# Kernel optimization log

Hardware: AMD Instinct MI355X
Metric: run time of the kernel (lower is better)

The kernel has to match this reference:

```python
import jax, jax.numpy as jnp
import numpy as np

N, M, D = 1024, 1024, 512


def setup_inputs() -> dict:
    key = jax.random.key(0)
    ks = jax.random.split(key, 12)
    s = 1.0 / np.sqrt(D)
    return {
        "q": jax.random.normal(ks[0], (N, D), jnp.float32),
        "k": jax.random.normal(ks[1], (M, D), jnp.float32),
        "v": jax.random.normal(ks[2], (M, D), jnp.float32),
        "mask": jax.random.randint(ks[3], (N, M), 0, 2) > 0,
        "Wq": jax.random.normal(ks[4], (D, D), jnp.float32) * s,
        "bq": jax.random.normal(ks[5], (D,), jnp.float32) * s,
        "Wk": jax.random.normal(ks[6], (D, D), jnp.float32) * s,
        "bk": jax.random.normal(ks[7], (D,), jnp.float32) * s,
        "Wv": jax.random.normal(ks[8], (D, D), jnp.float32) * s,
        "bv": jax.random.normal(ks[9], (D,), jnp.float32) * s,
        "Ww": jax.random.normal(ks[10], (D,), jnp.float32) * s,
        "bw": jax.random.normal(ks[11], (1,), jnp.float32) * s,
    }


def reference(q, k, v, mask, Wq, bq, Wk, bk, Wv, bv, Ww, bw):
    # Linear projections (torch Linear: x @ W.T + b)
    qp = q @ Wq.T + bq  # [N, D]
    kp = k @ Wk.T + bk  # [M, D]
    vp = v @ Wv.T + bv  # [M, D]
    # Bahdanau additive score: W(tanh(q_n + k_m)) -> [N, M]
    h = jnp.tanh(qp[:, None, :] + kp[None, :, :])  # [N, M, D]
    scores = jnp.einsum('nmd,d->nm', h, Ww) + bw[0]
    scores = jnp.where(mask, scores, jnp.float32(-1000000.0))
    attn = jax.nn.softmax(scores, axis=1)  # softmax over M (dim 1)
    context = jnp.einsum('nm,md->nd', attn, vp)  # [N, D]
    return context
```

## Files before the change

kernel.cpp:

```cpp
#include <hip/hip_runtime.h>
#include <hip/hip_bf16.h>
#include <float.h>


#define NROWS 1024
#define DDIM  512
#define MDIM  1024

typedef __attribute__((ext_vector_type(8))) short s8v;
typedef __attribute__((ext_vector_type(4))) float f4v;
typedef __attribute__((ext_vector_type(2))) float v2f;

__device__ __forceinline__ float bf2f(ushort h) {
    return __uint_as_float(((unsigned)h) << 16);
}
__device__ __forceinline__ ushort2 f2bf2(float a, float b) {
    __hip_bfloat162 t = __float22bfloat162_rn(float2{a, b});
    union { __hip_bfloat162 v; ushort2 u; } c; c.v = t;
    return c.u;
}
__device__ __forceinline__ void hl2(float a, float b, ushort2& h, ushort2& l) {
    h = f2bf2(a, b);
    l = f2bf2(a - bf2f(h.x), b - bf2f(h.y));
}

__global__ __launch_bounds__(256) void proj_gemm(
    const float* __restrict__ q, const float* __restrict__ kk_,
    const float* __restrict__ v,
    const float* __restrict__ Wq, const float* __restrict__ bq,
    const float* __restrict__ Wk, const float* __restrict__ bk,
    const float* __restrict__ Wv, const float* __restrict__ bv,
    float* __restrict__ eq, float* __restrict__ ekT,
    ushort* __restrict__ vph, ushort* __restrict__ vpl,
    float* __restrict__ rsum, float CS)
{
    __shared__ ushort Ah[2][4096], Al[2][4096], Bh[2][2048], Bl[2][2048];

    const float* A; const float* B; const float* bias;
    int biasRow;
    if (blockIdx.z == 0)      { A = q;   B = Wq;  bias = bq; biasRow = 0; }
    else if (blockIdx.z == 1) { A = Wk;  B = kk_; bias = bk; biasRow = 1; }
    else                      { A = Wv;  B = v;   bias = bv; biasRow = 1; }

    const int bx = blockIdx.x;
    const int bi = (blockIdx.z == 0) ? (bx >> 4) : (bx >> 5);
    const int bj = (blockIdx.z == 0) ? (bx & 15) : (bx & 31);

    const int t    = threadIdx.x;
    const int lane = t & 63;
    const int w    = t >> 6;
    const int lm   = lane & 15;
    const int lq   = lane >> 4;
    const int i0   = bi * 64;
    const int j0   = bj * 32;
    const int mh   = (w >> 1) * 32;
    const int nh   = (w & 1) * 16;

    if (blockIdx.z == 0 && bx == 0) {
        float4 zz = {0.f, 0.f, 0.f, 0.f};
        *(float4*)&rsum[t * 4] = zz;
    }

    const int sr = t >> 4, sc4 = t & 15;

    float4 pa[4], pb[2];

#define LOAD_CHUNK(KC)                                                         \
    {                                                                          \
        const int k0 = (KC) * 64;                                              \
        _Pragma("unroll")                                                      \
        for (int p = 0; p < 4; ++p)                                            \
            pa[p] = *(const float4*)&A[(size_t)(i0 + sr + p * 16) * DDIM       \
                                       + k0 + sc4 * 4];                        \
        _Pragma("unroll")                                                      \
        for (int p = 0; p < 2; ++p)                                            \
            pb[p] = *(const float4*)&B[(size_t)(j0 + sr + p * 16) * DDIM       \
                                       + k0 + sc4 * 4];                        \
    }

#define WRITE_CHUNK(BUF)                                                       \
    {                                                                          \
        _Pragma("unroll")                                                      \
        for (int p = 0; p < 4; ++p) {                                          \
            int r = sr + p * 16;                                               \
            int ad = r * 64 + (((sc4 >> 1) ^ (r & 7)) << 3) + (sc4 & 1) * 4;   \
            ushort2 h01, l01, h23, l23;                                        \
            hl2(pa[p].x, pa[p].y, h01, l01);                                   \
            hl2(pa[p].z, pa[p].w, h23, l23);                                   \
            ushort4 ha = {h01.x, h01.y, h23.x, h23.y};                         \
            ushort4 la = {l01.x, l01.y, l23.x, l23.y};                         \
            *(ushort4*)&Ah[BUF][ad] = ha;                                      \
            *(ushort4*)&Al[BUF][ad] = la;                                      \
        }                                                                      \
        _Pragma("unroll")                                                      \
        for (int p = 0; p < 2; ++p) {                                          \
            int r = sr + p * 16;                                               \
            int ad = r * 64 + (((sc4 >> 1) ^ (r & 7)) << 3) + (sc4 & 1) * 4;   \
            ushort2 h01, l01, h23, l23;                                        \
            hl2(pb[p].x, pb[p].y, h01, l01);                                   \
            hl2(pb[p].z, pb[p].w, h23, l23);                                   \
            ushort4 hb = {h01.x, h01.y, h23.x, h23.y};                         \
            ushort4 lb = {l01.x, l01.y, l23.x, l23.y};                         \
            *(ushort4*)&Bh[BUF][ad] = hb;                                      \
            *(ushort4*)&Bl[BUF][ad] = lb;                                      \
        }                                                                      \
    }

    f4v acc[2] = {{0.f,0.f,0.f,0.f},{0.f,0.f,0.f,0.f}};

    LOAD_CHUNK(0)
    WRITE_CHUNK(0)
    LOAD_CHUNK(1)
    __syncthreads();

    for (int kc = 0; kc < 8; ++kc) {
        const int buf = kc & 1;
#pragma unroll
        for (int ks = 0; ks < 2; ++ks) {
            const int kb = ks * 4 + lq;
            s8v afh[2], afl[2], bfh, bfl;
#pragma unroll
            for (int g = 0; g < 2; ++g) {
                int ra = mh + g * 16 + lm;
                int aa = ra * 64 + ((kb ^ (ra & 7)) << 3);
                afh[g] = *(const s8v*)&Ah[buf][aa];
                afl[g] = *(const s8v*)&Al[buf][aa];
            }
            {
                int rb = nh + lm;
                int ab = rb * 64 + ((kb ^ (rb & 7)) << 3);
                bfh = *(const s8v*)&Bh[buf][ab];
                bfl = *(const s8v*)&Bl[buf][ab];
            }
#pragma unroll
            for (int mi = 0; mi < 2; ++mi) {
                acc[mi] = __builtin_amdgcn_mfma_f32_16x16x32_bf16(
                    afh[mi], bfh, acc[mi], 0, 0, 0);
                acc[mi] = __builtin_amdgcn_mfma_f32_16x16x32_bf16(
                    afh[mi], bfl, acc[mi], 0, 0, 0);
                acc[mi] = __builtin_amdgcn_mfma_f32_16x16x32_bf16(
                    afl[mi], bfh, acc[mi], 0, 0, 0);
            }
        }
        if (kc < 7) {
            WRITE_CHUNK(buf ^ 1)
        }
        if (kc < 6) {
            LOAD_CHUNK(kc + 2)
        }
        __syncthreads();
    }

    const float CLAMP = 8192.0f;
    const float SCw   = 1.220703125e-4f;
#pragma unroll
    for (int mi = 0; mi < 2; ++mi) {
#pragma unroll
        for (int p = 0; p < 4; ++p) {
            int row = i0 + mh + mi * 16 + lq * 4 + p;
            int col = j0 + nh + lm;
            float val = acc[mi][p] + (biasRow ? bias[row] : bias[col]);
            if (blockIdx.z == 0) {
                eq[(size_t)row * 512 + col] =
                    fminf(__builtin_amdgcn_exp2f(val * CS), CLAMP) * SCw;
            } else if (blockIdx.z == 1) {
                ekT[(size_t)row * 1024 + col] =
                    fminf(__builtin_amdgcn_exp2f(val * CS), CLAMP);
            } else {
                ushort2 h2 = f2bf2(val, val);
                vph[(size_t)row * 1024 + col] = h2.x;
                ushort2 l2 = f2bf2(val - bf2f(h2.x), 0.f);
                vpl[(size_t)row * 1024 + col] = l2.x;
            }
        }
    }
#undef LOAD_CHUNK
#undef WRITE_CHUNK
}


#define TREE8(K0,K1,K2,K3,K4,K5,K6,K7,DCQ)                                     \
    {                                                                          \
        float4 wgA = *(const float4*)&wws[(DCQ)];                              \
        float4 wgB = *(const float4*)&wws[(DCQ) + 4];                          \
        _Pragma("unroll")                                                      \
        for (int nn = 0; nn < 4; ++nn) {                                       \
            float4 egA = *(const float4*)&es[nn * 512 + (DCQ)];                \
            float4 egB = *(const float4*)&es[nn * 512 + (DCQ) + 4];            \
            v2f A0 = __builtin_elementwise_fma(K0, (v2f){egA.x, egA.x}, cc2);  \
            v2f A1 = __builtin_elementwise_fma(K1, (v2f){egA.y, egA.y}, cc2);  \
            v2f A2 = __builtin_elementwise_fma(K2, (v2f){egA.z, egA.z}, cc2);  \
            v2f A3 = __builtin_elementwise_fma(K3, (v2f){egA.w, egA.w}, cc2);  \
            v2f A4 = __builtin_elementwise_fma(K4, (v2f){egB.x, egB.x}, cc2);  \
            v2f A5 = __builtin_elementwise_fma(K5, (v2f){egB.y, egB.y}, cc2);  \
            v2f A6 = __builtin_elementwise_fma(K6, (v2f){egB.z, egB.z}, cc2);  \
            v2f A7 = __builtin_elementwise_fma(K7, (v2f){egB.w, egB.w}, cc2);  \
            v2f n01 = __builtin_elementwise_fma((v2f){wgA.y, wgA.y}, A0,       \
                                                (v2f){wgA.x, wgA.x} * A1);     \
            v2f d01 = A0 * A1;                                                 \
            v2f n23 = __builtin_elementwise_fma((v2f){wgA.w, wgA.w}, A2,       \
                                                (v2f){wgA.z, wgA.z} * A3);     \
            v2f d23 = A2 * A3;                                                 \
            v2f n45 = __builtin_elementwise_fma((v2f){wgB.y, wgB.y}, A4,       \
                                                (v2f){wgB.x, wgB.x} * A5);     \
            v2f d45 = A4 * A5;                                                 \
            v2f n67 = __builtin_elementwise_fma((v2f){wgB.w, wgB.w}, A6,       \
                                                (v2f){wgB.z, wgB.z} * A7);     \
            v2f d67 = A6 * A7;                                                 \
            v2f nA = __builtin_elementwise_fma(n01, d23, n23 * d01);           \
            v2f dA = d01 * d23;                                                \
            v2f nB = __builtin_elementwise_fma(n45, d67, n67 * d45);           \
            v2f dB = d45 * d67;                                                \
            v2f num = __builtin_elementwise_fma(nA, dB, nB * dA);              \
            v2f den = dA * dB;                                                 \
            v2f r = {__builtin_amdgcn_rcpf(den.x),                             \
                     __builtin_amdgcn_rcpf(den.y)};                            \
            acc[nn] = __builtin_elementwise_fma(num, r, acc[nn]);              \
        }                                                                      \
    }

__global__ __launch_bounds__(256) void score_kernel(const float* __restrict__ eq,
                                                    const float* __restrict__ ekT,
                                                    const float* __restrict__ Ww,
                                                    const int* __restrict__ mask,
                                                    ushort* __restrict__ Ph,
                                                    ushort* __restrict__ Pl,
                                                    float* __restrict__ rsum)
{
    __shared__ __align__(16) float es[4 * 512];
    __shared__ __align__(16) float wws[512];
    const int t    = threadIdx.x;
    const int lane = t & 63;
    const int w    = t >> 6;
    const int mw   = blockIdx.x * 512 + w * 128;
    const int n0   = blockIdx.y * 4;

    const float SC = 1.220703125e-4f;

#pragma unroll
    for (int p = 0; p < 2; ++p) {
        int idx = t + p * 256;
        int nl = idx >> 7, c4 = idx & 127;
        *(float4*)&es[nl * 512 + c4 * 4] =
            *(const float4*)&eq[(size_t)(n0 + nl) * DDIM + c4 * 4];
    }
    wws[t]       = Ww[t] * SC;
    wws[t + 256] = Ww[t + 256] * SC;

    const float* gk = ekT + mw + lane * 2;

    v2f a0 = *(const v2f*)(gk + (size_t)0 * MDIM);
    v2f a1 = *(const v2f*)(gk + (size_t)1 * MDIM);
    v2f a2 = *(const v2f*)(gk + (size_t)2 * MDIM);
    v2f a3 = *(const v2f*)(gk + (size_t)3 * MDIM);
    v2f a4 = *(const v2f*)(gk + (size_t)4 * MDIM);
    v2f a5 = *(const v2f*)(gk + (size_t)5 * MDIM);
    v2f a6 = *(const v2f*)(gk + (size_t)6 * MDIM);
    v2f a7 = *(const v2f*)(gk + (size_t)7 * MDIM);

    __syncthreads();

    v2f acc[4] = {};
    const v2f cc2 = {1.220703125e-4f, 1.220703125e-4f};

    for (int dc = 0; dc < 512; dc += 16) {
        const float* g8 = gk + (size_t)(dc + 8) * MDIM;
        v2f b0 = *(const v2f*)(g8 + (size_t)0 * MDIM);
        v2f b1 = *(const v2f*)(g8 + (size_t)1 * MDIM);
        v2f b2 = *(const v2f*)(g8 + (size_t)2 * MDIM);
        v2f b3 = *(const v2f*)(g8 + (size_t)3 * MDIM);
        v2f b4 = *(const v2f*)(g8 + (size_t)4 * MDIM);
        v2f b5 = *(const v2f*)(g8 + (size_t)5 * MDIM);
        v2f b6 = *(const v2f*)(g8 + (size_t)6 * MDIM);
        v2f b7 = *(const v2f*)(g8 + (size_t)7 * MDIM);

        TREE8(a0, a1, a2, a3, a4, a5, a6, a7, dc)

        if (dc + 16 < 512) {
            const float* g16 = gk + (size_t)(dc + 16) * MDIM;
            a0 = *(const v2f*)(g16 + (size_t)0 * MDIM);
            a1 = *(const v2f*)(g16 + (size_t)1 * MDIM);
            a2 = *(const v2f*)(g16 + (size_t)2 * MDIM);
            a3 = *(const v2f*)(g16 + (size_t)3 * MDIM);
            a4 = *(const v2f*)(g16 + (size_t)4 * MDIM);
            a5 = *(const v2f*)(g16 + (size_t)5 * MDIM);
            a6 = *(const v2f*)(g16 + (size_t)6 * MDIM);
            a7 = *(const v2f*)(g16 + (size_t)7 * MDIM);
        }

        TREE8(b0, b1, b2, b3, b4, b5, b6, b7, dc + 8)
    }

    const float C2 = -2.8853900817779268f;
    const int m = mw + lane * 2;
    float rs[4];
#pragma unroll
    for (int nn = 0; nn < 4; ++nn) {
        int n = n0 + nn;
        int2 mk = *(const int2*)&mask[(size_t)n * MDIM + m];
        float p0 = mk.x ? __builtin_amdgcn_exp2f(acc[nn].x * C2) : 0.f;
        float p1 = mk.y ? __builtin_amdgcn_exp2f(acc[nn].y * C2) : 0.f;
        ushort2 h, l;
        hl2(p0, p1, h, l);
        *(ushort2*)&Ph[(size_t)n * MDIM + m] = h;
        *(ushort2*)&Pl[(size_t)n * MDIM + m] = l;
        rs[nn] = p0 + p1;
    }
#pragma unroll
    for (int off = 32; off; off >>= 1) {
        rs[0] += __shfl_xor(rs[0], off);
        rs[1] += __shfl_xor(rs[1], off);
        rs[2] += __shfl_xor(rs[2], off);
        rs[3] += __shfl_xor(rs[3], off);
    }
    if (lane == 0) {
#pragma unroll
        for (int nn = 0; nn < 4; ++nn)
            atomicAdd(&rsum[n0 + nn], rs[nn]);
    }
}

__global__ __launch_bounds__(256) void ctx_gemm(const ushort* __restrict__ Ph,
                                                const ushort* __restrict__ Pl,
                                                const ushort* __restrict__ vph,
                                                const ushort* __restrict__ vpl,
                                                const float* __restrict__ rsum,
                                                float* __restrict__ out)
{
    __shared__ __align__(16) float red[3 * 64 * 4];
    const int t    = threadIdx.x;
    const int lane = t & 63;
    const int w    = t >> 6;
    const int lm   = lane & 15;
    const int lq   = lane >> 4;
    const int d0   = blockIdx.x * 16;
    const int n0   = blockIdx.y * 16;
    const int mb   = w * 256;

    const ushort* pAh = Ph  + (size_t)(n0 + lm) * MDIM + mb + lq * 8;
    const ushort* pAl = Pl  + (size_t)(n0 + lm) * MDIM + mb + lq * 8;
    const ushort* pBh = vph + (size_t)(d0 + lm) * MDIM + mb + lq * 8;
    const ushort* pBl = vpl + (size_t)(d0 + lm) * MDIM + mb + lq * 8;

    f4v acc = {0.f, 0.f, 0.f, 0.f};
#pragma unroll 4
    for (int m0 = 0; m0 < 256; m0 += 32) {
        s8v ah = *(const s8v*)(pAh + m0);
        s8v al = *(const s8v*)(pAl + m0);
        s8v bh = *(const s8v*)(pBh + m0);
        s8v bl = *(const s8v*)(pBl + m0);
        acc = __builtin_amdgcn_mfma_f32_16x16x32_bf16(ah, bh, acc, 0, 0, 0);
        acc = __builtin_amdgcn_mfma_f32_16x16x32_bf16(ah, bl, acc, 0, 0, 0);
        acc = __builtin_amdgcn_mfma_f32_16x16x32_bf16(al, bh, acc, 0, 0, 0);
    }

    if (w > 0) *(f4v*)&red[((w - 1) * 64 + lane) * 4] = acc;
    __syncthreads();
    if (w == 0) {
#pragma unroll
        for (int i = 0; i < 3; ++i)
            acc += *(const f4v*)&red[(i * 64 + lane) * 4];
#pragma unroll
        for (int p = 0; p < 4; ++p) {
            int nrow = n0 + lq * 4 + p;
            float inv = __builtin_amdgcn_rcpf(rsum[nrow]);
            out[(size_t)nrow * DDIM + d0 + lm] = acc[p] * inv;
        }
    }
}

extern "C" void kernel_launch(void* const* d_in, const int* in_sizes, int n_in,
                              void* d_out, int out_size, void* d_ws, size_t ws_size,
                              hipStream_t stream)
{
    const float* q    = (const float*)d_in[0];
    const float* k    = (const float*)d_in[1];
    const float* v    = (const float*)d_in[2];
    const int*   mask = (const int*)d_in[3];
    const float* Wq   = (const float*)d_in[4];
    const float* bq   = (const float*)d_in[5];
    const float* Wk   = (const float*)d_in[6];
    const float* bk   = (const float*)d_in[7];
    const float* Wv   = (const float*)d_in[8];
    const float* bv   = (const float*)d_in[9];
    const float* Ww   = (const float*)d_in[10];

    float* ws    = (float*)d_ws;
    float* eq    = ws;
    float* ekT   = ws + 524288;
    ushort* vph  = (ushort*)(ws + 1048576);
    ushort* vpl  = (ushort*)(ws + 1310720);
    ushort* Ph   = (ushort*)(ws + 1572864);
    ushort* Pl   = (ushort*)(ws + 2097152);
    float* rsum  = ws + 2621440;
    float* out   = (float*)d_out;

    const float CS = 2.8853900817779268f;

    proj_gemm<<<dim3(256, 1, 3), dim3(256), 0, stream>>>(q, k, v, Wq, bq, Wk, bk,
                                                         Wv, bv, eq, ekT,
                                                         vph, vpl, rsum, CS);
    score_kernel<<<dim3(2, 256), dim3(256), 0, stream>>>(eq, ekT, Ww, mask,
                                                         Ph, Pl, rsum);
    ctx_gemm<<<dim3(32, 64), dim3(256), 0, stream>>>(Ph, Pl, vph, vpl, rsum, out);
}
```

Baseline: 175.8 us.

## Split D reduction across two wave groups in score kernel with LDS combine

The score kernel now launches 512 threads per block. Two groups of four waves each handle half of the D dimension for the same m columns, and their partial accumulators are combined through shared memory before the exp, mask and store epilogue. This doubles the waves per block and halves the serial reduction loop per thread, aiming for more latency hiding in the score computation. It costs an extra LDS buffer, a block-wide barrier, and half the waves idling during the epilogue.

Result: no change. 172.9 us (-1.6%).

```diff
diff --git a/kernel.cpp b/kernel.cpp
--- a/kernel.cpp
+++ b/kernel.cpp
@@ -219,7 +219,7 @@
         }                                                                      \
     }
 
-__global__ __launch_bounds__(256) void score_kernel(const float* __restrict__ eq,
+__global__ __launch_bounds__(512) void score_kernel(const float* __restrict__ eq,
                                                     const float* __restrict__ ekT,
                                                     const float* __restrict__ Ww,
                                                     const int* __restrict__ mask,
@@ -229,25 +229,26 @@
 {
     __shared__ __align__(16) float es[4 * 512];
     __shared__ __align__(16) float wws[512];
+    __shared__ __align__(16) float red[4 * 8 * 64];
     const int t    = threadIdx.x;
     const int lane = t & 63;
     const int w    = t >> 6;
-    const int mw   = blockIdx.x * 512 + w * 128;
+    const int mg   = w & 3;
+    const int dh   = w >> 2;
+    const int mw   = blockIdx.x * 512 + mg * 128;
     const int n0   = blockIdx.y * 4;
+    const int db   = dh * 256;
 
     const float SC = 1.220703125e-4f;
 
-#pragma unroll
-    for (int p = 0; p < 2; ++p) {
-        int idx = t + p * 256;
-        int nl = idx >> 7, c4 = idx & 127;
+    {
+        int nl = t >> 7, c4 = t & 127;
         *(float4*)&es[nl * 512 + c4 * 4] =
             *(const float4*)&eq[(size_t)(n0 + nl) * DDIM + c4 * 4];
     }
-    wws[t]       = Ww[t] * SC;
-    wws[t + 256] = Ww[t + 256] * SC;
-
-    const float* gk = ekT + mw + lane * 2;
+    wws[t] = Ww[t] * SC;
+
+    const float* gk = ekT + (size_t)db * MDIM + mw + lane * 2;
 
     v2f a0 = *(const v2f*)(gk + (size_t)0 * MDIM);
     v2f a1 = *(const v2f*)(gk + (size_t)1 * MDIM);
@@ -263,7 +264,7 @@
     v2f acc[4] = {};
     const v2f cc2 = {1.220703125e-4f, 1.220703125e-4f};
 
-    for (int dc = 0; dc < 512; dc += 16) {
+    for (int dc = 0; dc < 256; dc += 16) {
         const float* g8 = gk + (size_t)(dc + 8) * MDIM;
         v2f b0 = *(const v2f*)(g8 + (size_t)0 * MDIM);
         v2f b1 = *(const v2f*)(g8 + (size_t)1 * MDIM);
@@ -274,9 +275,9 @@
         v2f b6 = *(const v2f*)(g8 + (size_t)6 * MDIM);
         v2f b7 = *(const v2f*)(g8 + (size_t)7 * MDIM);
 
-        TREE8(a0, a1, a2, a3, a4, a5, a6, a7, dc)
-
-        if (dc + 16 < 512) {
+        TREE8(a0, a1, a2, a3, a4, a5, a6, a7, db + dc)
+
+        if (dc + 16 < 256) {
             const float* g16 = gk + (size_t)(dc + 16) * MDIM;
             a0 = *(const v2f*)(g16 + (size_t)0 * MDIM);
             a1 = *(const v2f*)(g16 + (size_t)1 * MDIM);
@@ -288,35 +289,51 @@
             a7 = *(const v2f*)(g16 + (size_t)7 * MDIM);
         }
 
-        TREE8(b0, b1, b2, b3, b4, b5, b6, b7, dc + 8)
-    }
-
-    const float C2 = -2.8853900817779268f;
-    const int m = mw + lane * 2;
-    float rs[4];
-#pragma unroll
-    for (int nn = 0; nn < 4; ++nn) {
-        int n = n0 + nn;
-        int2 mk = *(const int2*)&mask[(size_t)n * MDIM + m];
-        float p0 = mk.x ? __builtin_amdgcn_exp2f(acc[nn].x * C2) : 0.f;
-        float p1 = mk.y ? __builtin_amdgcn_exp2f(acc[nn].y * C2) : 0.f;
-        ushort2 h, l;
-        hl2(p0, p1, h, l);
-        *(ushort2*)&Ph[(size_t)n * MDIM + m] = h;
-        *(ushort2*)&Pl[(size_t)n * MDIM + m] = l;
-        rs[nn] = p0 + p1;
-    }
-#pragma unroll
-    for (int off = 32; off; off >>= 1) {
-        rs[0] += __shfl_xor(rs[0], off);
-        rs[1] += __shfl_xor(rs[1], off);
-        rs[2] += __shfl_xor(rs[2], off);
-        rs[3] += __shfl_xor(rs[3], off);
-    }
-    if (lane == 0) {
-#pragma unroll
-        for (int nn = 0; nn < 4; ++nn)
-            atomicAdd(&rsum[n0 + nn], rs[nn]);
+        TREE8(b0, b1, b2, b3, b4, b5, b6, b7, db + dc + 8)
+    }
+
+    if (dh) {
+        float* rb = &red[(mg * 8) * 64 + lane];
+        rb[0 * 64] = acc[0].x; rb[1 * 64] = acc[0].y;
+        rb[2 * 64] = acc[1].x; rb[3 * 64] = acc[1].y;
+        rb[4 * 64] = acc[2].x; rb[5 * 64] = acc[2].y;
+        rb[6 * 64] = acc[3].x; rb[7 * 64] = acc[3].y;
+    }
+    __syncthreads();
+    if (!dh) {
+        const float* rb = &red[(mg * 8) * 64 + lane];
+        acc[0].x += rb[0 * 64]; acc[0].y += rb[1 * 64];
+        acc[1].x += rb[2 * 64]; acc[1].y += rb[3 * 64];
+        acc[2].x += rb[4 * 64]; acc[2].y += rb[5 * 64];
+        acc[3].x += rb[6 * 64]; acc[3].y += rb[7 * 64];
+
+        const float C2 = -2.8853900817779268f;
+        const int m = mw + lane * 2;
+        float rs[4];
+#pragma unroll
+        for (int nn = 0; nn < 4; ++nn) {
+            int n = n0 + nn;
+            int2 mk = *(const int2*)&mask[(size_t)n * MDIM + m];
+            float p0 = mk.x ? __builtin_amdgcn_exp2f(acc[nn].x * C2) : 0.f;
+            float p1 = mk.y ? __builtin_amdgcn_exp2f(acc[nn].y * C2) : 0.f;
+            ushort2 h, l;
+            hl2(p0, p1, h, l);
+            *(ushort2*)&Ph[(size_t)n * MDIM + m] = h;
+            *(ushort2*)&Pl[(size_t)n * MDIM + m] = l;
+            rs[nn] = p0 + p1;
+        }
+#pragma unroll
+        for (int off = 32; off; off >>= 1) {
+            rs[0] += __shfl_xor(rs[0], off);
+            rs[1] += __shfl_xor(rs[1], off);
+            rs[2] += __shfl_xor(rs[2], off);
+            rs[3] += __shfl_xor(rs[3], off);
+        }
+        if (lane == 0) {
+#pragma unroll
+            for (int nn = 0; nn < 4; ++nn)
+                atomicAdd(&rsum[n0 + nn], rs[nn]);
+        }
     }
 }
 
@@ -400,7 +417,7 @@
     proj_gemm<<<dim3(256, 1, 3), dim3(256), 0, stream>>>(q, k, v, Wq, bq, Wk, bk,
                                                          Wv, bv, eq, ekT,
                                                          vph, vpl, rsum, CS);
-    score_kernel<<<dim3(2, 256), dim3(256), 0, stream>>>(eq, ekT, Ww, mask,
+    score_kernel<<<dim3(2, 256), dim3(512), 0, stream>>>(eq, ekT, Ww, mask,
                                                          Ph, Pl, rsum);
     ctx_gemm<<<dim3(32, 64), dim3(256), 0, stream>>>(Ph, Pl, vph, vpl, rsum, out);
 }
```

## Split score kernel D reduction across wave pairs with 4-wide m per lane

Applied to the files above, without the earlier changes.

Each wave now computes 4 adjacent m columns per lane (float4 loads of ekT) over half of the D dimension, and two waves covering the same m range combine partial sums through shared memory before the mask/exp/store epilogue. This doubles per-lane register tiling, so each broadcast es/wws value read from LDS feeds more FMAs and the reads per useful op drop. The cost is higher register pressure from f4v accumulators and operands, an extra block barrier and LDS reduction, and half the waves sitting idle during the epilogue.

After: 169.1 us (median of 2 runs). 1.04x faster.

```diff
diff --git a/kernel.cpp b/kernel.cpp
--- a/kernel.cpp
+++ b/kernel.cpp
@@ -179,7 +179,7 @@
 }
 
 
-#define TREE8(K0,K1,K2,K3,K4,K5,K6,K7,DCQ)                                     \
+#define TREE8_F4(K0,K1,K2,K3,K4,K5,K6,K7,DCQ)                                  \
     {                                                                          \
         float4 wgA = *(const float4*)&wws[(DCQ)];                              \
         float4 wgB = *(const float4*)&wws[(DCQ) + 4];                          \
@@ -187,34 +187,48 @@
         for (int nn = 0; nn < 4; ++nn) {                                       \
             float4 egA = *(const float4*)&es[nn * 512 + (DCQ)];                \
             float4 egB = *(const float4*)&es[nn * 512 + (DCQ) + 4];            \
-            v2f A0 = __builtin_elementwise_fma(K0, (v2f){egA.x, egA.x}, cc2);  \
-            v2f A1 = __builtin_elementwise_fma(K1, (v2f){egA.y, egA.y}, cc2);  \
-            v2f A2 = __builtin_elementwise_fma(K2, (v2f){egA.z, egA.z}, cc2);  \
-            v2f A3 = __builtin_elementwise_fma(K3, (v2f){egA.w, egA.w}, cc2);  \
-            v2f A4 = __builtin_elementwise_fma(K4, (v2f){egB.x, egB.x}, cc2);  \
-            v2f A5 = __builtin_elementwise_fma(K5, (v2f){egB.y, egB.y}, cc2);  \
-            v2f A6 = __builtin_elementwise_fma(K6, (v2f){egB.z, egB.z}, cc2);  \
-            v2f A7 = __builtin_elementwise_fma(K7, (v2f){egB.w, egB.w}, cc2);  \
-            v2f n01 = __builtin_elementwise_fma((v2f){wgA.y, wgA.y}, A0,       \
-                                                (v2f){wgA.x, wgA.x} * A1);     \
-            v2f d01 = A0 * A1;                                                 \
-            v2f n23 = __builtin_elementwise_fma((v2f){wgA.w, wgA.w}, A2,       \
-                                                (v2f){wgA.z, wgA.z} * A3);     \
-            v2f d23 = A2 * A3;                                                 \
-            v2f n45 = __builtin_elementwise_fma((v2f){wgB.y, wgB.y}, A4,       \
-                                                (v2f){wgB.x, wgB.x} * A5);     \
-            v2f d45 = A4 * A5;                                                 \
-            v2f n67 = __builtin_elementwise_fma((v2f){wgB.w, wgB.w}, A6,       \
-                                                (v2f){wgB.z, wgB.z} * A7);     \
-            v2f d67 = A6 * A7;                                                 \
-            v2f nA = __builtin_elementwise_fma(n01, d23, n23 * d01);           \
-            v2f dA = d01 * d23;                                                \
-            v2f nB = __builtin_elementwise_fma(n45, d67, n67 * d45);           \
-            v2f dB = d45 * d67;                                                \
-            v2f num = __builtin_elementwise_fma(nA, dB, nB * dA);              \
-            v2f den = dA * dB;                                                 \
-            v2f r = {__builtin_amdgcn_rcpf(den.x),                             \
-                     __builtin_amdgcn_rcpf(den.y)};                            \
+            f4v A0 = __builtin_elementwise_fma(K0,                             \
+                     (f4v){egA.x, egA.x, egA.x, egA.x}, cc4);                  \
+            f4v A1 = __builtin_elementwise_fma(K1,                             \
+                     (f4v){egA.y, egA.y, egA.y, egA.y}, cc4);                  \
+            f4v A2 = __builtin_elementwise_fma(K2,                             \
+                     (f4v){egA.z, egA.z, egA.z, egA.z}, cc4);                  \
+            f4v A3 = __builtin_elementwise_fma(K3,                             \
+                     (f4v){egA.w, egA.w, egA.w, egA.w}, cc4);                  \
+            f4v A4 = __builtin_elementwise_fma(K4,                             \
+                     (f4v){egB.x, egB.x, egB.x, egB.x}, cc4);                  \
+            f4v A5 = __builtin_elementwise_fma(K5,                             \
+                     (f4v){egB.y, egB.y, egB.y, egB.y}, cc4);                  \
+            f4v A6 = __builtin_elementwise_fma(K6,                             \
+                     (f4v){egB.z, egB.z, egB.z, egB.z}, cc4);                  \
+            f4v A7 = __builtin_elementwise_fma(K7,                             \
+                     (f4v){egB.w, egB.w, egB.w, egB.w}, cc4);                  \
+            f4v n01 = __builtin_elementwise_fma(                               \
+                (f4v){wgA.y, wgA.y, wgA.y, wgA.y}, A0,                         \
+                (f4v){wgA.x, wgA.x, wgA.x, wgA.x} * A1);                       \
+            f4v d01 = A0 * A1;                                                 \
+            f4v n23 = __builtin_elementwise_fma(                               \
+                (f4v){wgA.w, wgA.w, wgA.w, wgA.w}, A2,                         \
+                (f4v){wgA.z, wgA.z, wgA.z, wgA.z} * A3);                       \
+            f4v d23 = A2 * A3;                                                 \
+            f4v n45 = __builtin_elementwise_fma(                               \
+                (f4v){wgB.y, wgB.y, wgB.y, wgB.y}, A4,                         \
+                (f4v){wgB.x, wgB.x, wgB.x, wgB.x} * A5);                       \
+            f4v d45 = A4 * A5;                                                 \
+            f4v n67 = __builtin_elementwise_fma(                               \
+                (f4v){wgB.w, wgB.w, wgB.w, wgB.w}, A6,                         \
+                (f4v){wgB.z, wgB.z, wgB.z, wgB.z} * A7);                       \
+            f4v d67 = A6 * A7;                                                 \
+            f4v nA = __builtin_elementwise_fma(n01, d23, n23 * d01);           \
+            f4v dA = d01 * d23;                                                \
+            f4v nB = __builtin_elementwise_fma(n45, d67, n67 * d45);           \
+            f4v dB = d45 * d67;                                                \
+            f4v num = __builtin_elementwise_fma(nA, dB, nB * dA);              \
+            f4v den = dA * dB;                                                 \
+            f4v r = {__builtin_amdgcn_rcpf(den.x),                             \
+                     __builtin_amdgcn_rcpf(den.y),                             \
+                     __builtin_amdgcn_rcpf(den.z),                             \
+                     __builtin_amdgcn_rcpf(den.w)};                            \
             acc[nn] = __builtin_elementwise_fma(num, r, acc[nn]);              \
         }                                                                      \
     }
@@ -229,11 +243,15 @@
 {
     __shared__ __align__(16) float es[4 * 512];
     __shared__ __align__(16) float wws[512];
+    __shared__ __align__(16) float red[2 * 16 * 64];
     const int t    = threadIdx.x;
     const int lane = t & 63;
     const int w    = t >> 6;
-    const int mw   = blockIdx.x * 512 + w * 128;
+    const int mg   = w & 1;
+    const int dh   = w >> 1;
+    const int mw   = blockIdx.x * 512 + mg * 256;
     const int n0   = blockIdx.y * 4;
+    const int db   = dh * 256;
 
     const float SC = 1.220703125e-4f;
 
@@ -247,76 +265,104 @@
     wws[t]       = Ww[t] * SC;
     wws[t + 256] = Ww[t + 256] * SC;
 
-    const float* gk = ekT + mw + lane * 2;
-
-    v2f a0 = *(const v2f*)(gk + (size_t)0 * MDIM);
-    v2f a1 = *(const v2f*)(gk + (size_t)1 * MDIM);
-    v2f a2 = *(const v2f*)(gk + (size_t)2 * MDIM);
-    v2f a3 = *(const v2f*)(gk + (size_t)3 * MDIM);
-    v2f a4 = *(const v2f*)(gk + (size_t)4 * MDIM);
-    v2f a5 = *(const v2f*)(gk + (size_t)5 * MDIM);
-    v2f a6 = *(const v2f*)(gk + (size_t)6 * MDIM);
-    v2f a7 = *(const v2f*)(gk + (size_t)7 * MDIM);
+    const float* gk = ekT + (size_t)db * MDIM + mw + lane * 4;
+
+    f4v a0 = *(const f4v*)(gk + (size_t)0 * MDIM);
+    f4v a1 = *(const f4v*)(gk + (size_t)1 * MDIM);
+    f4v a2 = *(const f4v*)(gk + (size_t)2 * MDIM);
+    f4v a3 = *(const f4v*)(gk + (size_t)3 * MDIM);
+    f4v a4 = *(const f4v*)(gk + (size_t)4 * MDIM);
+    f4v a5 = *(const f4v*)(gk + (size_t)5 * MDIM);
+    f4v a6 = *(const f4v*)(gk + (size_t)6 * MDIM);
+    f4v a7 = *(const f4v*)(gk + (size_t)7 * MDIM);
 
     __syncthreads();
 
-    v2f acc[4] = {};
-    const v2f cc2 = {1.220703125e-4f, 1.220703125e-4f};
-
-    for (int dc = 0; dc < 512; dc += 16) {
+    f4v acc[4] = {};
+    const f4v cc4 = {1.220703125e-4f, 1.220703125e-4f,
+                     1.220703125e-4f, 1.220703125e-4f};
+
+    for (int dc = 0; dc < 256; dc += 16) {
         const float* g8 = gk + (size_t)(dc + 8) * MDIM;
-        v2f b0 = *(const v2f*)(g8 + (size_t)0 * MDIM);
-        v2f b1 = *(const v2f*)(g8 + (size_t)1 * MDIM);
-        v2f b2 = *(const v2f*)(g8 + (size_t)2 * MDIM);
-        v2f b3 = *(const v2f*)(g8 + (size_t)3 * MDIM);
-        v2f b4 = *(const v2f*)(g8 + (size_t)4 * MDIM);
-        v2f b5 = *(const v2f*)(g8 + (size_t)5 * MDIM);
-        v2f b6 = *(const v2f*)(g8 + (size_t)6 * MDIM);
-        v2f b7 = *(const v2f*)(g8 + (size_t)7 * MDIM);
-
-        TREE8(a0, a1, a2, a3, a4, a5, a6, a7, dc)
-
-        if (dc + 16 < 512) {
+        f4v b0 = *(const f4v*)(g8 + (size_t)0 * MDIM);
+        f4v b1 = *(const f4v*)(g8 + (size_t)1 * MDIM);
+        f4v b2 = *(const f4v*)(g8 + (size_t)2 * MDIM);
+        f4v b3 = *(const f4v*)(g8 + (size_t)3 * MDIM);
+        f4v b4 = *(const f4v*)(g8 + (size_t)4 * MDIM);
+        f4v b5 = *(const f4v*)(g8 + (size_t)5 * MDIM);
+        f4v b6 = *(const f4v*)(g8 + (size_t)6 * MDIM);
+        f4v b7 = *(const f4v*)(g8 + (size_t)7 * MDIM);
+
+        TREE8_F4(a0, a1, a2, a3, a4, a5, a6, a7, db + dc)
+
+        if (dc + 16 < 256) {
             const float* g16 = gk + (size_t)(dc + 16) * MDIM;
-            a0 = *(const v2f*)(g16 + (size_t)0 * MDIM);
-            a1 = *(const v2f*)(g16 + (size_t)1 * MDIM);
-            a2 = *(const v2f*)(g16 + (size_t)2 * MDIM);
-            a3 = *(const v2f*)(g16 + (size_t)3 * MDIM);
-            a4 = *(const v2f*)(g16 + (size_t)4 * MDIM);
-            a5 = *(const v2f*)(g16 + (size_t)5 * MDIM);
-            a6 = *(const v2f*)(g16 + (size_t)6 * MDIM);
-            a7 = *(const v2f*)(g16 + (size_t)7 * MDIM);
-        }
-
-        TREE8(b0, b1, b2, b3, b4, b5, b6, b7, dc + 8)
-    }
-
-    const float C2 = -2.8853900817779268f;
-    const int m = mw + lane * 2;
-    float rs[4];
-#pragma unroll
-    for (int nn = 0; nn < 4; ++nn) {
-        int n = n0 + nn;
-        int2 mk = *(const int2*)&mask[(size_t)n * MDIM + m];
-        float p0 = mk.x ? __builtin_amdgcn_exp2f(acc[nn].x * C2) : 0.f;
-        float p1 = mk.y ? __builtin_amdgcn_exp2f(acc[nn].y * C2) : 0.f;
-        ushort2 h, l;
-        hl2(p0, p1, h, l);
-        *(ushort2*)&Ph[(size_t)n * MDIM + m] = h;
-        *(ushort2*)&Pl[(size_t)n * MDIM + m] = l;
-        rs[nn] = p0 + p1;
-    }
-#pragma unroll
-    for (int off = 32; off; off >>= 1) {
-        rs[0] += __shfl_xor(rs[0], off);
-        rs[1] += __shfl_xor(rs[1], off);
-        rs[2] += __shfl_xor(rs[2], off);
-        rs[3] += __shfl_xor(rs[3], off);
-    }
-    if (lane == 0) {
-#pragma unroll
-        for (int nn = 0; nn < 4; ++nn)
-            atomicAdd(&rsum[n0 + nn], rs[nn]);
+            a0 = *(const f4v*)(g16 + (size_t)0 * MDIM);
+            a1 = *(const f4v*)(g16 + (size_t)1 * MDIM);
+            a2 = *(const f4v*)(g16 + (size_t)2 * MDIM);
+            a3 = *(const f4v*)(g16 + (size_t)3 * MDIM);
+            a4 = *(const f4v*)(g16 + (size_t)4 * MDIM);
+            a5 = *(const f4v*)(g16 + (size_t)5 * MDIM);
+            a6 = *(const f4v*)(g16 + (size_t)6 * MDIM);
+            a7 = *(const f4v*)(g16 + (size_t)7 * MDIM);
+        }
+
+        TREE8_F4(b0, b1, b2, b3, b4, b5, b6, b7, db + dc + 8)
+    }
+
+    if (dh) {
+        float* rb = &red[(mg * 16) * 64 + lane];
+#pragma unroll
+        for (int nn = 0; nn < 4; ++nn) {
+            rb[(nn * 4 + 0) * 64] = acc[nn].x;
+            rb[(nn * 4 + 1) * 64] = acc[nn].y;
+            rb[(nn * 4 + 2) * 64] = acc[nn].z;
+            rb[(nn * 4 + 3) * 64] = acc[nn].w;
+        }
+    }
+    __syncthreads();
+    if (!dh) {
+        const float* rb = &red[(mg * 16) * 64 + lane];
+#pragma unroll
+        for (int nn = 0; nn < 4; ++nn) {
+            acc[nn].x += rb[(nn * 4 + 0) * 64];
+            acc[nn].y += rb[(nn * 4 + 1) * 64];
+            acc[nn].z += rb[(nn * 4 + 2) * 64];
+            acc[nn].w += rb[(nn * 4 + 3) * 64];
+        }
+
+        const float C2 = -2.8853900817779268f;
+        const int m = mw + lane * 4;
+        float rs[4];
+#pragma unroll
+        for (int nn = 0; nn < 4; ++nn) {
+            int n = n0 + nn;
+            int4 mk = *(const int4*)&mask[(size_t)n * MDIM + m];
+            float p0 = mk.x ? __builtin_amdgcn_exp2f(acc[nn].x * C2) : 0.f;
+            float p1 = mk.y ? __builtin_amdgcn_exp2f(acc[nn].y * C2) : 0.f;
+            float p2 = mk.z ? __builtin_amdgcn_exp2f(acc[nn].z * C2) : 0.f;
+            float p3 = mk.w ? __builtin_amdgcn_exp2f(acc[nn].w * C2) : 0.f;
+            ushort2 h01, l01, h23, l23;
+            hl2(p0, p1, h01, l01);
+            hl2(p2, p3, h23, l23);
+            ushort4 hv = {h01.x, h01.y, h23.x, h23.y};
+            ushort4 lv = {l01.x, l01.y, l23.x, l23.y};
+            *(ushort4*)&Ph[(size_t)n * MDIM + m] = hv;
+            *(ushort4*)&Pl[(size_t)n * MDIM + m] = lv;
+            rs[nn] = (p0 + p1) + (p2 + p3);
+        }
+#pragma unroll
+        for (int off = 32; off; off >>= 1) {
+            rs[0] += __shfl_xor(rs[0], off);
+            rs[1] += __shfl_xor(rs[1], off);
+            rs[2] += __shfl_xor(rs[2], off);
+            rs[3] += __shfl_xor(rs[3], off);
+        }
+        if (lane == 0) {
+#pragma unroll
+            for (int nn = 0; nn < 4; ++nn)
+                atomicAdd(&rsum[n0 + nn], rs[nn]);
+        }
     }
 }
 
```

## Split score kernel reduction over D across waves with LDS cross-wave reduction

Applied to the files above, without the earlier changes.

Each wave in the score kernel now covers all 512 M columns of the block (8 per lane, as float4 pairs) but only a quarter of the D dimension, instead of 128 columns over all of D. Partial accumulators from waves 1-3 are reduced through a new 24 KB shared buffer into wave 0, which alone applies the mask, exp, bf16 split and row-sum atomics. The aim is wider vector loads of ekT and a shorter serial loop per wave. The cost is more registers per lane, an extra barrier and LDS round trip, and an epilogue that runs on only one wave in four.

After: 181.6 us. +3.3%, slower.

```diff
diff --git a/kernel.cpp b/kernel.cpp
--- a/kernel.cpp
+++ b/kernel.cpp
@@ -179,7 +179,8 @@
 }
 
 
-#define TREE8(K0,K1,K2,K3,K4,K5,K6,K7,DCQ)                                     \
+#define TREE16(KL0,KL1,KL2,KL3,KL4,KL5,KL6,KL7,                                \
+               KH0,KH1,KH2,KH3,KH4,KH5,KH6,KH7,DCQ)                            \
     {                                                                          \
         float4 wgA = *(const float4*)&wws[(DCQ)];                              \
         float4 wgB = *(const float4*)&wws[(DCQ) + 4];                          \
@@ -187,37 +188,88 @@
         for (int nn = 0; nn < 4; ++nn) {                                       \
             float4 egA = *(const float4*)&es[nn * 512 + (DCQ)];                \
             float4 egB = *(const float4*)&es[nn * 512 + (DCQ) + 4];            \
-            v2f A0 = __builtin_elementwise_fma(K0, (v2f){egA.x, egA.x}, cc2);  \
-            v2f A1 = __builtin_elementwise_fma(K1, (v2f){egA.y, egA.y}, cc2);  \
-            v2f A2 = __builtin_elementwise_fma(K2, (v2f){egA.z, egA.z}, cc2);  \
-            v2f A3 = __builtin_elementwise_fma(K3, (v2f){egA.w, egA.w}, cc2);  \
-            v2f A4 = __builtin_elementwise_fma(K4, (v2f){egB.x, egB.x}, cc2);  \
-            v2f A5 = __builtin_elementwise_fma(K5, (v2f){egB.y, egB.y}, cc2);  \
-            v2f A6 = __builtin_elementwise_fma(K6, (v2f){egB.z, egB.z}, cc2);  \
-            v2f A7 = __builtin_elementwise_fma(K7, (v2f){egB.w, egB.w}, cc2);  \
-            v2f n01 = __builtin_elementwise_fma((v2f){wgA.y, wgA.y}, A0,       \
-                                                (v2f){wgA.x, wgA.x} * A1);     \
-            v2f d01 = A0 * A1;                                                 \
-            v2f n23 = __builtin_elementwise_fma((v2f){wgA.w, wgA.w}, A2,       \
-                                                (v2f){wgA.z, wgA.z} * A3);     \
-            v2f d23 = A2 * A3;                                                 \
-            v2f n45 = __builtin_elementwise_fma((v2f){wgB.y, wgB.y}, A4,       \
-                                                (v2f){wgB.x, wgB.x} * A5);     \
-            v2f d45 = A4 * A5;                                                 \
-            v2f n67 = __builtin_elementwise_fma((v2f){wgB.w, wgB.w}, A6,       \
-                                                (v2f){wgB.z, wgB.z} * A7);     \
-            v2f d67 = A6 * A7;                                                 \
-            v2f nA = __builtin_elementwise_fma(n01, d23, n23 * d01);           \
-            v2f dA = d01 * d23;                                                \
-            v2f nB = __builtin_elementwise_fma(n45, d67, n67 * d45);           \
-            v2f dB = d45 * d67;                                                \
-            v2f num = __builtin_elementwise_fma(nA, dB, nB * dA);              \
-            v2f den = dA * dB;                                                 \
-            v2f r = {__builtin_amdgcn_rcpf(den.x),                             \
-                     __builtin_amdgcn_rcpf(den.y)};                            \
-            acc[nn] = __builtin_elementwise_fma(num, r, acc[nn]);              \
+            f4v eA0 = {egA.x, egA.x, egA.x, egA.x};                            \
+            f4v eA1 = {egA.y, egA.y, egA.y, egA.y};                            \
+            f4v eA2 = {egA.z, egA.z, egA.z, egA.z};                            \
+            f4v eA3 = {egA.w, egA.w, egA.w, egA.w};                            \
+            f4v eB0 = {egB.x, egB.x, egB.x, egB.x};                            \
+            f4v eB1 = {egB.y, egB.y, egB.y, egB.y};                            \
+            f4v eB2 = {egB.z, egB.z, egB.z, egB.z};                            \
+            f4v eB3 = {egB.w, egB.w, egB.w, egB.w};                            \
+            f4v wA0 = {wgA.x, wgA.x, wgA.x, wgA.x};                            \
+            f4v wA1 = {wgA.y, wgA.y, wgA.y, wgA.y};                            \
+            f4v wA2 = {wgA.z, wgA.z, wgA.z, wgA.z};                            \
+            f4v wA3 = {wgA.w, wgA.w, wgA.w, wgA.w};                            \
+            f4v wB0 = {wgB.x, wgB.x, wgB.x, wgB.x};                            \
+            f4v wB1 = {wgB.y, wgB.y, wgB.y, wgB.y};                            \
+            f4v wB2 = {wgB.z, wgB.z, wgB.z, wgB.z};                            \
+            f4v wB3 = {wgB.w, wgB.w, wgB.w, wgB.w};                            \
+                                                         \
+            {                                                                  \
+                f4v A0 = __builtin_elementwise_fma(KL0, eA0, cc4);             \
+                f4v A1 = __builtin_elementwise_fma(KL1, eA1, cc4);             \
+                f4v A2 = __builtin_elementwise_fma(KL2, eA2, cc4);             \
+                f4v A3 = __builtin_elementwise_fma(KL3, eA3, cc4);             \
+                f4v A4 = __builtin_elementwise_fma(KL4, eB0, cc4);             \
+                f4v A5 = __builtin_elementwise_fma(KL5, eB1, cc4);             \
+                f4v A6 = __builtin_elementwise_fma(KL6, eB2, cc4);             \
+                f4v A7 = __builtin_elementwise_fma(KL7, eB3, cc4);             \
+                f4v n01 = __builtin_elementwise_fma(wA1, A0, wA0 * A1);        \
+                f4v d01 = A0 * A1;                                             \
+                f4v n23 = __builtin_elementwise_fma(wA3, A2, wA2 * A3);        \
+                f4v d23 = A2 * A3;                                             \
+                f4v n45 = __builtin_elementwise_fma(wB1, A4, wB0 * A5);        \
+                f4v d45 = A4 * A5;                                             \
+                f4v n67 = __builtin_elementwise_fma(wB3, A6, wB2 * A7);        \
+                f4v d67 = A6 * A7;                                             \
+                f4v nA = __builtin_elementwise_fma(n01, d23, n23 * d01);       \
+                f4v dA = d01 * d23;                                            \
+                f4v nB = __builtin_elementwise_fma(n45, d67, n67 * d45);       \
+                f4v dB = d45 * d67;                                            \
+                f4v num = __builtin_elementwise_fma(nA, dB, nB * dA);          \
+                f4v den = dA * dB;                                             \
+                f4v r = {__builtin_amdgcn_rcpf(den.x),                         \
+                         __builtin_amdgcn_rcpf(den.y),                         \
+                         __builtin_amdgcn_rcpf(den.z),                         \
+                         __builtin_amdgcn_rcpf(den.w)};                        \
+                accL[nn] = __builtin_elementwise_fma(num, r, accL[nn]);        \
+            }                                                                  \
+                                                         \
+            {                                                                  \
+                f4v A0 = __builtin_elementwise_fma(KH0, eA0, cc4);             \
+                f4v A1 = __builtin_elementwise_fma(KH1, eA1, cc4);             \
+                f4v A2 = __builtin_elementwise_fma(KH2, eA2, cc4);             \
+                f4v A3 = __builtin_elementwise_fma(KH3, eA3, cc4);             \
+                f4v A4 = __builtin_elementwise_fma(KH4, eB0, cc4);             \
+                f4v A5 = __builtin_elementwise_fma(KH5, eB1, cc4);             \
+                f4v A6 = __builtin_elementwise_fma(KH6, eB2, cc4);             \
+                f4v A7 = __builtin_elementwise_fma(KH7, eB3, cc4);             \
+                f4v n01 = __builtin_elementwise_fma(wA1, A0, wA0 * A1);        \
+                f4v d01 = A0 * A1;                                             \
+                f4v n23 = __builtin_elementwise_fma(wA3, A2, wA2 * A3);        \
+                f4v d23 = A2 * A3;                                             \
+                f4v n45 = __builtin_elementwise_fma(wB1, A4, wB0 * A5);        \
+                f4v d45 = A4 * A5;                                             \
+                f4v n67 = __builtin_elementwise_fma(wB3, A6, wB2 * A7);        \
+                f4v d67 = A6 * A7;                                             \
+                f4v nA = __builtin_elementwise_fma(n01, d23, n23 * d01);       \
+                f4v dA = d01 * d23;                                            \
+                f4v nB = __builtin_elementwise_fma(n45, d67, n67 * d45);       \
+                f4v dB = d45 * d67;                                            \
+                f4v num = __builtin_elementwise_fma(nA, dB, nB * dA);          \
+                f4v den = dA * dB;                                             \
+                f4v r = {__builtin_amdgcn_rcpf(den.x),                         \
+                         __builtin_amdgcn_rcpf(den.y),                         \
+                         __builtin_amdgcn_rcpf(den.z),                         \
+                         __builtin_amdgcn_rcpf(den.w)};                        \
+                accH[nn] = __builtin_elementwise_fma(num, r, accH[nn]);        \
+            }                                                                  \
         }                                                                      \
     }
+
+#define LOADK(DST_L, DST_H, ROWPTR)                                            \
+    DST_L = *(const f4v*)(ROWPTR);                                             \
+    DST_H = *(const f4v*)((ROWPTR) + 4);
 
 __global__ __launch_bounds__(256) void score_kernel(const float* __restrict__ eq,
                                                     const float* __restrict__ ekT,
@@ -229,11 +281,13 @@
 {
     __shared__ __align__(16) float es[4 * 512];
     __shared__ __align__(16) float wws[512];
+    __shared__ __align__(16) float red[3 * 32 * 64];
     const int t    = threadIdx.x;
     const int lane = t & 63;
     const int w    = t >> 6;
-    const int mw   = blockIdx.x * 512 + w * 128;
+    const int mw   = blockIdx.x * 512;
     const int n0   = blockIdx.y * 4;
+    const int db   = w * 128;
 
     const float SC = 1.220703125e-4f;
 
@@ -247,76 +301,132 @@
     wws[t]       = Ww[t] * SC;
     wws[t + 256] = Ww[t + 256] * SC;
 
-    const float* gk = ekT + mw + lane * 2;
-
-    v2f a0 = *(const v2f*)(gk + (size_t)0 * MDIM);
-    v2f a1 = *(const v2f*)(gk + (size_t)1 * MDIM);
-    v2f a2 = *(const v2f*)(gk + (size_t)2 * MDIM);
-    v2f a3 = *(const v2f*)(gk + (size_t)3 * MDIM);
-    v2f a4 = *(const v2f*)(gk + (size_t)4 * MDIM);
-    v2f a5 = *(const v2f*)(gk + (size_t)5 * MDIM);
-    v2f a6 = *(const v2f*)(gk + (size_t)6 * MDIM);
-    v2f a7 = *(const v2f*)(gk + (size_t)7 * MDIM);
+    const float* gk = ekT + (size_t)db * MDIM + mw + lane * 8;
+
+    f4v aL0, aH0, aL1, aH1, aL2, aH2, aL3, aH3;
+    f4v aL4, aH4, aL5, aH5, aL6, aH6, aL7, aH7;
+    LOADK(aL0, aH0, gk + (size_t)0 * MDIM)
+    LOADK(aL1, aH1, gk + (size_t)1 * MDIM)
+    LOADK(aL2, aH2, gk + (size_t)2 * MDIM)
+    LOADK(aL3, aH3, gk + (size_t)3 * MDIM)
+    LOADK(aL4, aH4, gk + (size_t)4 * MDIM)
+    LOADK(aL5, aH5, gk + (size_t)5 * MDIM)
+    LOADK(aL6, aH6, gk + (size_t)6 * MDIM)
+    LOADK(aL7, aH7, gk + (size_t)7 * MDIM)
 
     __syncthreads();
 
-    v2f acc[4] = {};
-    const v2f cc2 = {1.220703125e-4f, 1.220703125e-4f};
-
-    for (int dc = 0; dc < 512; dc += 16) {
+    f4v accL[4] = {}, accH[4] = {};
+    const f4v cc4 = {1.220703125e-4f, 1.220703125e-4f,
+                     1.220703125e-4f, 1.220703125e-4f};
+
+    for (int dc = 0; dc < 128; dc += 16) {
         const float* g8 = gk + (size_t)(dc + 8) * MDIM;
-        v2f b0 = *(const v2f*)(g8 + (size_t)0 * MDIM);
-        v2f b1 = *(const v2f*)(g8 + (size_t)1 * MDIM);
-        v2f b2 = *(const v2f*)(g8 + (size_t)2 * MDIM);
-        v2f b3 = *(const v2f*)(g8 + (size_t)3 * MDIM);
-        v2f b4 = *(const v2f*)(g8 + (size_t)4 * MDIM);
-        v2f b5 = *(const v2f*)(g8 + (size_t)5 * MDIM);
-        v2f b6 = *(const v2f*)(g8 + (size_t)6 * MDIM);
-        v2f b7 = *(const v2f*)(g8 + (size_t)7 * MDIM);
-
-        TREE8(a0, a1, a2, a3, a4, a5, a6, a7, dc)
-
-        if (dc + 16 < 512) {
+        f4v bL0, bH0, bL1, bH1, bL2, bH2, bL3, bH3;
+        f4v bL4, bH4, bL5, bH5, bL6, bH6, bL7, bH7;
+        LOADK(bL0, bH0, g8 + (size_t)0 * MDIM)
+        LOADK(bL1, bH1, g8 + (size_t)1 * MDIM)
+        LOADK(bL2, bH2, g8 + (size_t)2 * MDIM)
+        LOADK(bL3, bH3, g8 + (size_t)3 * MDIM)
+        LOADK(bL4, bH4, g8 + (size_t)4 * MDIM)
+        LOADK(bL5, bH5, g8 + (size_t)5 * MDIM)
+        LOADK(bL6, bH6, g8 + (size_t)6 * MDIM)
+        LOADK(bL7, bH7, g8 + (size_t)7 * MDIM)
+
+        TREE16(aL0, aL1, aL2, aL3, aL4, aL5, aL6, aL7,
+               aH0, aH1, aH2, aH3, aH4, aH5, aH6, aH7, db + dc)
+
+        if (dc + 16 < 128) {
             const float* g16 = gk + (size_t)(dc + 16) * MDIM;
-            a0 = *(const v2f*)(g16 + (size_t)0 * MDIM);
-            a1 = *(const v2f*)(g16 + (size_t)1 * MDIM);
-            a2 = *(const v2f*)(g16 + (size_t)2 * MDIM);
-            a3 = *(const v2f*)(g16 + (size_t)3 * MDIM);
-            a4 = *(const v2f*)(g16 + (size_t)4 * MDIM);
-            a5 = *(const v2f*)(g16 + (size_t)5 * MDIM);
-            a6 = *(const v2f*)(g16 + (size_t)6 * MDIM);
-            a7 = *(const v2f*)(g16 + (size_t)7 * MDIM);
-        }
-
-        TREE8(b0, b1, b2, b3, b4, b5, b6, b7, dc + 8)
-    }
-
-    const float C2 = -2.8853900817779268f;
-    const int m = mw + lane * 2;
-    float rs[4];
-#pragma unroll
-    for (int nn = 0; nn < 4; ++nn) {
-        int n = n0 + nn;
-        int2 mk = *(const int2*)&mask[(size_t)n * MDIM + m];
-        float p0 = mk.x ? __builtin_amdgcn_exp2f(acc[nn].x * C2) : 0.f;
-        float p1 = mk.y ? __builtin_amdgcn_exp2f(acc[nn].y * C2) : 0.f;
-        ushort2 h, l;
-        hl2(p0, p1, h, l);
-        *(ushort2*)&Ph[(size_t)n * MDIM + m] = h;
-        *(ushort2*)&Pl[(size_t)n * MDIM + m] = l;
-        rs[nn] = p0 + p1;
-    }
-#pragma unroll
-    for (int off = 32; off; off >>= 1) {
-        rs[0] += __shfl_xor(rs[0], off);
-        rs[1] += __shfl_xor(rs[1], off);
-        rs[2] += __shfl_xor(rs[2], off);
-        rs[3] += __shfl_xor(rs[3], off);
-    }
-    if (lane == 0) {
-#pragma unroll
-        for (int nn = 0; nn < 4; ++nn)
-            atomicAdd(&rsum[n0 + nn], rs[nn]);
+            LOADK(aL0, aH0, g16 + (size_t)0 * MDIM)
+            LOADK(aL1, aH1, g16 + (size_t)1 * MDIM)
+            LOADK(aL2, aH2, g16 + (size_t)2 * MDIM)
+            LOADK(aL3, aH3, g16 + (size_t)3 * MDIM)
+            LOADK(aL4, aH4, g16 + (size_t)4 * MDIM)
+            LOADK(aL5, aH5, g16 + (size_t)5 * MDIM)
+            LOADK(aL6, aH6, g16 + (size_t)6 * MDIM)
+            LOADK(aL7, aH7, g16 + (size_t)7 * MDIM)
+        }
+
+        TREE16(bL0, bL1, bL2, bL3, bL4, bL5, bL6, bL7,
+               bH0, bH1, bH2, bH3, bH4, bH5, bH6, bH7, db + dc + 8)
+    }
+
+    if (w > 0) {
+        float* rb = &red[((w - 1) * 32) * 64 + lane];
+#pragma unroll
+        for (int nn = 0; nn < 4; ++nn) {
+            rb[(nn * 8 + 0) * 64] = accL[nn].x;
+            rb[(nn * 8 + 1) * 64] = accL[nn].y;
+            rb[(nn * 8 + 2) * 64] = accL[nn].z;
+            rb[(nn * 8 + 3) * 64] = accL[nn].w;
+            rb[(nn * 8 + 4) * 64] = accH[nn].x;
+            rb[(nn * 8 + 5) * 64] = accH[nn].y;
+            rb[(nn * 8 + 6) * 64] = accH[nn].z;
+            rb[(nn * 8 + 7) * 64] = accH[nn].w;
+        }
+    }
+    __syncthreads();
+    if (w == 0) {
+#pragma unroll
+        for (int i = 0; i < 3; ++i) {
+            const float* rb = &red[(i * 32) * 64 + lane];
+#pragma unroll
+            for (int nn = 0; nn < 4; ++nn) {
+                accL[nn].x += rb[(nn * 8 + 0) * 64];
+                accL[nn].y += rb[(nn * 8 + 1) * 64];
+                accL[nn].z += rb[(nn * 8 + 2) * 64];
+                accL[nn].w += rb[(nn * 8 + 3) * 64];
+                accH[nn].x += rb[(nn * 8 + 4) * 64];
+                accH[nn].y += rb[(nn * 8 + 5) * 64];
+                accH[nn].z += rb[(nn * 8 + 6) * 64];
+                accH[nn].w += rb[(nn * 8 + 7) * 64];
+            }
+        }
+
+        const float C2 = -2.8853900817779268f;
+        const int m = mw + lane * 8;
+        float rs[4];
+#pragma unroll
+        for (int nn = 0; nn < 4; ++nn) {
+            int n = n0 + nn;
+            int4 mkL = *(const int4*)&mask[(size_t)n * MDIM + m];
+            int4 mkH = *(const int4*)&mask[(size_t)n * MDIM + m + 4];
+            float p0 = mkL.x ? __builtin_amdgcn_exp2f(accL[nn].x * C2) : 0.f;
+            float p1 = mkL.y ? __builtin_amdgcn_exp2f(accL[nn].y * C2) : 0.f;
+            float p2 = mkL.z ? __builtin_amdgcn_exp2f(accL[nn].z * C2) : 0.f;
+            float p3 = mkL.w ? __builtin_amdgcn_exp2f(accL[nn].w * C2) : 0.f;
+            float p4 = mkH.x ? __builtin_amdgcn_exp2f(accH[nn].x * C2) : 0.f;
+            float p5 = mkH.y ? __builtin_amdgcn_exp2f(accH[nn].y * C2) : 0.f;
+            float p6 = mkH.z ? __builtin_amdgcn_exp2f(accH[nn].z * C2) : 0.f;
+            float p7 = mkH.w ? __builtin_amdgcn_exp2f(accH[nn].w * C2) : 0.f;
+            ushort2 h01, l01, h23, l23, h45, l45, h67, l67;
+            hl2(p0, p1, h01, l01);
+            hl2(p2, p3, h23, l23);
+            hl2(p4, p5, h45, l45);
+            hl2(p6, p7, h67, l67);
+            ushort4 hvL = {h01.x, h01.y, h23.x, h23.y};
+            ushort4 lvL = {l01.x, l01.y, l23.x, l23.y};
+            ushort4 hvH = {h45.x, h45.y, h67.x, h67.y};
+            ushort4 lvH = {l45.x, l45.y, l67.x, l67.y};
+            *(ushort4*)&Ph[(size_t)n * MDIM + m]     = hvL;
+            *(ushort4*)&Pl[(size_t)n * MDIM + m]     = lvL;
+            *(ushort4*)&Ph[(size_t)n * MDIM + m + 4] = hvH;
+            *(ushort4*)&Pl[(size_t)n * MDIM + m + 4] = lvH;
+            rs[nn] = ((p0 + p1) + (p2 + p3)) + ((p4 + p5) + (p6 + p7));
+        }
+#pragma unroll
+        for (int off = 32; off; off >>= 1) {
+            rs[0] += __shfl_xor(rs[0], off);
+            rs[1] += __shfl_xor(rs[1], off);
+            rs[2] += __shfl_xor(rs[2], off);
+            rs[3] += __shfl_xor(rs[3], off);
+        }
+        if (lane == 0) {
+#pragma unroll
+            for (int nn = 0; nn < 4; ++nn)
+                atomicAdd(&rsum[n0 + nn], rs[nn]);
+        }
     }
 }
 
```
